# Performance work log

Measured on AMD Instinct MI355X. Metric: run time of the kernel, lower is better.

## Reference

```python
import jax, jax.numpy as jnp
import numpy as np

MODEL_DIM = 1024
NUM_HEADS = 16
D_K = MODEL_DIM // NUM_HEADS  # 64
MAX_SEQ_LEN = 3200
B, T = 2, 2048
THETA_BASE = 10000.0


def setup_inputs() -> dict:
    key = jax.random.key(0)
    ks = jax.random.split(key, 5)
    scale = 1.0 / np.sqrt(MODEL_DIM)
    x = jax.random.normal(ks[0], (B, T, MODEL_DIM), dtype=jnp.float32)
    wq = jax.random.normal(ks[1], (MODEL_DIM, MODEL_DIM), dtype=jnp.float32) * scale
    wk = jax.random.normal(ks[2], (MODEL_DIM, MODEL_DIM), dtype=jnp.float32) * scale
    wv = jax.random.normal(ks[3], (MODEL_DIM, MODEL_DIM), dtype=jnp.float32) * scale
    wo = jax.random.normal(ks[4], (MODEL_DIM, MODEL_DIM), dtype=jnp.float32) * scale
    bq = jnp.zeros((MODEL_DIM,), jnp.float32)
    bk = jnp.zeros((MODEL_DIM,), jnp.float32)
    bv = jnp.zeros((MODEL_DIM,), jnp.float32)
    bo = jnp.zeros((MODEL_DIM,), jnp.float32)
    # RoPE tables, exactly as precompute_rotation_matrix: theta duplicated
    # adjacently ([t0,t0,t1,t1,...]).
    theta = THETA_BASE ** (jnp.arange(D_K // 2, dtype=jnp.float32) * (-2.0 / D_K))
    ang = jnp.outer(jnp.arange(MAX_SEQ_LEN, dtype=jnp.float32), theta)  # [L, d/2]
    ang = jnp.repeat(ang, 2, axis=-1)  # [L, d]
    return {
        "x": x, "wq": wq, "bq": bq, "wk": wk, "bk": bk,
        "wv": wv, "bv": bv, "wo": wo, "bo": bo,
        "cos": jnp.cos(ang), "sin": jnp.sin(ang),
    }


def reference(x, wq, bq, wk, bk, wv, bv, wo, bo, cos, sin):
    b, t, dm = x.shape
    h, d = NUM_HEADS, dm // NUM_HEADS

    # NOTE: original uses .view(b, h, t, d) directly on [b, t, h*d] (no
    # transpose) — a nonstandard head split we replicate faithfully.
    xq = (x @ wq.T + bq).reshape(b, h, t, d)
    xk = (x @ wk.T + bk).reshape(b, h, t, d)
    xv = (x @ wv.T + bv).reshape(b, h, t, d)

    def rot_half(q):
        # pairs are adjacent (2i, 2i+1): out[2i] = -q[2i+1], out[2i+1] = q[2i]
        q2 = q.reshape(b, h, t, d // 2, 2)
        return jnp.stack([-q2[..., 1], q2[..., 0]], axis=-1).reshape(b, h, t, d)

    # NOTE: original indexes cos/sin at the single position `seq_len`
    # (rotation_matrix_cos[:, :, xq.shape[2], :]), broadcasting one row over
    # all positions — replicated faithfully.
    c = cos[t]  # [d]
    s = sin[t]  # [d]
    xq = xq * c + rot_half(xq) * s
    xk = xk * c + rot_half(xk) * s

    scores = jnp.einsum("bhqd,bhkd->bhqk", xq, xk) / np.sqrt(d)
    p = jax.nn.softmax(scores, axis=-1)  # mask='none', dropout=0.0
    o = jnp.einsum("bhqk,bhkd->bhqd", p, xv)
    o = o.transpose(0, 2, 1, 3).reshape(b, t, dm)  # 'b h t d -> b t (h d)'
    return o @ wo.T + bo
```

## Files before the change

### kernel.cpp

```cpp
#include <hip/hip_runtime.h>

typedef _Float16 half8 __attribute__((ext_vector_type(8)));
typedef __fp16 pkh2 __attribute__((ext_vector_type(2)));
typedef float floatx4 __attribute__((ext_vector_type(4)));

#define AS1 __attribute__((address_space(1)))
#define AS3 __attribute__((address_space(3)))


__global__ __launch_bounds__(256) void convert_kernel(
    const float* __restrict__ x, const float* __restrict__ wq,
    const float* __restrict__ wk, const float* __restrict__ wv,
    const float* __restrict__ wo,
    _Float16* __restrict__ xb, _Float16* __restrict__ wqkv,
    _Float16* __restrict__ wob)
{
    int i = (blockIdx.x * 256 + threadIdx.x) * 4;
    const float* src; _Float16* dst; int off;
    if (i < 4194304)      { src = x;  dst = xb;            off = i; }
    else if (i < 5242880) { src = wq; dst = wqkv;          off = i - 4194304; }
    else if (i < 6291456) { src = wk; dst = wqkv + 1048576; off = i - 5242880; }
    else if (i < 7340032) { src = wv; dst = wqkv + 2097152; off = i - 6291456; }
    else                  { src = wo; dst = wob;           off = i - 7340032; }
    float4 v = *(const float4*)(src + off);
    union { uint2 u; pkh2 h[2]; } o;
    o.h[0] = __builtin_amdgcn_cvt_pkrtz(v.x, v.y);
    o.h[1] = __builtin_amdgcn_cvt_pkrtz(v.z, v.w);
    *(uint2*)(dst + off) = o.u;
}

template<bool QKV, int BM, int BN>
__global__ __launch_bounds__(256) void gemm_kernel(
    const _Float16* __restrict__ A, const _Float16* __restrict__ W,
    const float* __restrict__ b0, const float* __restrict__ b1,
    const float* __restrict__ b2,
    const float* __restrict__ cosr, const float* __restrict__ sinr,
    _Float16* __restrict__ O0, _Float16* __restrict__ O1,
    _Float16* __restrict__ O2, float* __restrict__ Of)
{
    constexpr int MT   = (BN == 128) ? BM / 32 : BM / 64;
    constexpr int AISS = BM / 32;
    constexpr int WISS = BN / 32;
    __shared__ __align__(16) _Float16 As[BM * 64];
    __shared__ __align__(16) _Float16 Bs[BN * 64];
    const int tid  = threadIdx.x;
    const int lane = tid & 63, w = tid >> 6;
    const int lrow = lane & 15, quad = lane >> 4;
    const int wr = (BN == 128) ? (w & 1) * (BM / 2) : w * (BM / 4);
    const int wc = (BN == 128) ? (w >> 1) * 64 : 0;

    const int nwg  = gridDim.x * gridDim.y;
    const int flat = blockIdx.y * gridDim.x + blockIdx.x;
    const int idx  = (flat & 7) * (nwg >> 3) + (flat >> 3);
    const int bx   = idx % gridDim.x;
    const int by   = idx / gridDim.x;

    const int arow0 = bx * BM;
    const int brow0 = by * BN;

    const int r8 = lane >> 3;
    const int gcol = ((lane & 7) ^ r8) * 8;

    floatx4 acc[MT][4] = {};

    for (int kk = 0; kk < 1024; kk += 64) {
        __syncthreads();
        for (int u = 0; u < AISS; u++) {
            const int row = w * (8 * AISS) + u * 8;
            __builtin_amdgcn_global_load_lds(
                (const AS1 unsigned*)(const void*)(A + (size_t)(arow0 + row + r8) * 1024 + kk + gcol),
                (AS3 unsigned*)(void*)(As + row * 64), 16, 0, 0);
        }
        for (int u = 0; u < WISS; u++) {
            const int row = w * (8 * WISS) + u * 8;
            __builtin_amdgcn_global_load_lds(
                (const AS1 unsigned*)(const void*)(W + (size_t)(brow0 + row + r8) * 1024 + kk + gcol),
                (AS3 unsigned*)(void*)(Bs + row * 64), 16, 0, 0);
        }
        __syncthreads();
        for (int ks = 0; ks < 2; ks++) {
            const int swz = ((ks * 4 + quad) ^ (lrow & 7)) * 8;
            half8 af[MT], bf[4];
            for (int mt = 0; mt < MT; mt++)
                af[mt] = *(const half8*)&As[(wr + mt * 16 + lrow) * 64 + swz];
            for (int nt = 0; nt < 4; nt++)
                bf[nt] = *(const half8*)&Bs[(wc + nt * 16 + lrow) * 64 + swz];
            for (int mt = 0; mt < MT; mt++)
                for (int nt = 0; nt < 4; nt++)
                    acc[mt][nt] = __builtin_amdgcn_mfma_f32_16x16x32_f16(
                        af[mt], bf[nt], acc[mt][nt], 0, 0, 0);
        }
    }

    if (QKV) {
        constexpr int CTS = 1024 / BN;
        const int seg = by / CTS;
        const float* bias = seg == 0 ? b0 : (seg == 1 ? b1 : b2);
        _Float16* out = seg == 0 ? O0 : (seg == 1 ? O1 : O2);
        const int nbase = (by % CTS) * BN + wc;
        for (int nt = 0; nt < 4; nt++) {
            const int n = nbase + nt * 16 + lrow;
            const float bv = bias[n];
            const int dj = n & 63;
            const float cv = cosr[dj], sv = sinr[dj];
            const bool odd = (n & 1) != 0;
            const int ns = (seg == 1)
                ? ((n & ~56) | ((((n >> 3) ^ (n >> 6)) & 7) << 3))
                : n;
            for (int mt = 0; mt < MT; mt++)
                for (int r = 0; r < 4; r++) {
                    float v = acc[mt][nt][r] + bv;
                    if (seg < 2) {
                        float p = __shfl_xor(v, 1, 64);
                        v = odd ? (v * cv + p * sv) : (v * cv - p * sv);
                    }
                    if (seg == 0) v *= 0.125f;
                    int row = arow0 + wr + mt * 16 + quad * 4 + r;
                    out[row * 1024 + ns] = (_Float16)v;
                }
        }
    } else {
        const int nbase = by * BN + wc;
        for (int nt = 0; nt < 4; nt++) {
            const int n = nbase + nt * 16 + lrow;
            const float bv = b0[n];
            for (int mt = 0; mt < MT; mt++)
                for (int r = 0; r < 4; r++) {
                    int row = arow0 + wr + mt * 16 + quad * 4 + r;
                    Of[row * 1024 + n] = acc[mt][nt][r] + bv;
                }
        }
    }
}

__global__ __launch_bounds__(256) void vtrans_kernel(
    const _Float16* __restrict__ V, _Float16* __restrict__ VT)
{
    __shared__ __align__(16) _Float16 T[64][72];
    const int tid = threadIdx.x;
    const int kt = blockIdx.x;
    const int bh = blockIdx.y;
    const int bi = bh >> 4, hi = bh & 15;
    const _Float16* Vh = V + (size_t)(bi * 2048 + hi * 128) * 1024 + kt * 4096;
    const int srow = tid >> 3, sblk = tid & 7;
    union { uint4 u; _Float16 h[8]; } a, b;
    a.u = *(const uint4*)(Vh + (2 * srow) * 64 + sblk * 8);
    b.u = *(const uint4*)(Vh + (2 * srow + 1) * 64 + sblk * 8);
    for (int j = 0; j < 8; j++) {
        union { unsigned u; _Float16 h[2]; } pk;
        pk.h[0] = a.h[j]; pk.h[1] = b.h[j];
        *(unsigned*)&T[sblk * 8 + j][2 * srow] = pk.u;
    }
    __syncthreads();
    const int d = tid >> 2, c = tid & 3;
    const int xr = d & 7;
    _Float16* outrow = VT + ((size_t)bh * 64 + d) * 2048 + kt * 64;
    *(uint4*)(outrow + ((2 * c)     ^ xr) * 8) = *(const uint4*)&T[d][c * 16];
    *(uint4*)(outrow + ((2 * c + 1) ^ xr) * 8) = *(const uint4*)&T[d][c * 16 + 8];
}

static __device__ __forceinline__ half8 assemble_p(uint2 a, uint2 b) {
    auto s32x = __builtin_amdgcn_permlane32_swap(a.x, b.x, false, false);
    auto s32y = __builtin_amdgcn_permlane32_swap(a.y, b.y, false, false);
    auto s16x = __builtin_amdgcn_permlane16_swap(s32x[0], s32x[1], false, false);
    auto s16y = __builtin_amdgcn_permlane16_swap(s32y[0], s32y[1], false, false);
    union { uint4 u; half8 h; } r;
    r.u.x = s16x[0];
    r.u.y = s16y[0];
    r.u.z = s16x[1];
    r.u.w = s16y[1];
    return r.h;
}

__global__ __launch_bounds__(512, 4) void attn_kernel(
    const _Float16* __restrict__ Q, const _Float16* __restrict__ K,
    const _Float16* __restrict__ VT, _Float16* __restrict__ O)
{
    __shared__ __align__(16) _Float16 smem[32768];

    const int tid  = threadIdx.x;
    const int g    = tid >> 8;
    const int wg   = tid >> 6;
    const int w    = wg & 3;
    const int lane = tid & 63;
    const int lrow = lane & 15, quad = lane >> 4;

    const int bid = blockIdx.x;
    const int bh  = (bid & 7) * 4 + (bid >> 7);
    const int qt  = (bid >> 3) & 15;
    const int bi = bh >> 4, hi = bh & 15;
    const size_t base = (size_t)(bi * 2048 + hi * 128) * 1024;
    const _Float16* Qh  = Q + base;
    const _Float16* Kh  = K + base + (size_t)g * 65536;
    const _Float16* VTh = VT + (size_t)bh * 131072 + g * 1024;

    _Float16* Ks0  = smem + g * 16384;
    _Float16* Vts0 = smem + g * 16384 + 8192;

    half8 qf[2][2];
    for (int nt = 0; nt < 2; nt++)
        for (int ks = 0; ks < 2; ks++)
            qf[nt][ks] = *(const half8*)(Qh + (qt * 128 + w * 32 + nt * 16 + lrow) * 64
                                          + ks * 32 + quad * 8);

    floatx4 oacc[4][2] = {};
    float lsum0 = 0.0f, lsum1 = 0.0f;

    const _Float16* klsrc = Kh + w * 1024 + lane * 8;
    const _Float16* vlsrc = VTh + (size_t)(w * 16 + (lane >> 3)) * 2048 + (lane & 7) * 8;

    auto stage = [&](int kt, int b) {
        const _Float16* ks = klsrc + kt * 4096;
        _Float16* kd = Ks0 + b * 4096 + w * 1024;
        __builtin_amdgcn_global_load_lds((const AS1 unsigned*)(const void*)ks,
                                         (AS3 unsigned*)(void*)kd, 16, 0, 0);
        __builtin_amdgcn_global_load_lds((const AS1 unsigned*)(const void*)(ks + 512),
                                         (AS3 unsigned*)(void*)(kd + 512), 16, 0, 0);
        const _Float16* vs = vlsrc + kt * 64;
        _Float16* vd = Vts0 + b * 4096 + w * 1024;
        __builtin_amdgcn_global_load_lds((const AS1 unsigned*)(const void*)vs,
                                         (AS3 unsigned*)(void*)vd, 16, 0, 0);
        __builtin_amdgcn_global_load_lds((const AS1 unsigned*)(const void*)(vs + 8 * 2048),
                                         (AS3 unsigned*)(void*)(vd + 512), 16, 0, 0);
    };

    const float LOG2E = 1.44269504f;
    const float OFF   = -8.65617025f;

    stage(0, 0);
    __syncthreads();

    for (int ktl = 0; ktl < 16; ktl++) {
        const int cur = ktl & 1;
        if (ktl < 15) stage(ktl + 1, cur ^ 1);
        const _Float16* Ksg  = Ks0 + cur * 4096;
        const _Float16* Vtsg = Vts0 + cur * 4096;
        for (int h = 0; h < 2; h++) {
            union { uint2 u; pkh2 h2[2]; } pA[2], pB[2];
            for (int k2 = 0; k2 < 2; k2++) {
                const int kt4 = h * 2 + k2;
                floatx4 s0 = {}, s1 = {};
                __builtin_amdgcn_s_setprio(1);
                for (int ks = 0; ks < 2; ks++) {
                    half8 af = *(const half8*)&Ksg[(kt4 * 16 + lrow) * 64
                                 + (((ks * 4 + quad) ^ (lrow & 7)) * 8)];
                    s0 = __builtin_amdgcn_mfma_f32_16x16x32_f16(af, qf[0][ks], s0, 0, 0, 0);
                    s1 = __builtin_amdgcn_mfma_f32_16x16x32_f16(af, qf[1][ks], s1, 0, 0, 0);
                }
                __builtin_amdgcn_s_setprio(0);
                float p00 = __builtin_amdgcn_exp2f(fmaf(s0[0], LOG2E, OFF));
                float p01 = __builtin_amdgcn_exp2f(fmaf(s0[1], LOG2E, OFF));
                float p02 = __builtin_amdgcn_exp2f(fmaf(s0[2], LOG2E, OFF));
                float p03 = __builtin_amdgcn_exp2f(fmaf(s0[3], LOG2E, OFF));
                float p10 = __builtin_amdgcn_exp2f(fmaf(s1[0], LOG2E, OFF));
                float p11 = __builtin_amdgcn_exp2f(fmaf(s1[1], LOG2E, OFF));
                float p12 = __builtin_amdgcn_exp2f(fmaf(s1[2], LOG2E, OFF));
                float p13 = __builtin_amdgcn_exp2f(fmaf(s1[3], LOG2E, OFF));
                lsum0 += (p00 + p01) + (p02 + p03);
                lsum1 += (p10 + p11) + (p12 + p13);
                pA[k2].h2[0] = __builtin_amdgcn_cvt_pkrtz(p00, p01);
                pA[k2].h2[1] = __builtin_amdgcn_cvt_pkrtz(p02, p03);
                pB[k2].h2[0] = __builtin_amdgcn_cvt_pkrtz(p10, p11);
                pB[k2].h2[1] = __builtin_amdgcn_cvt_pkrtz(p12, p13);
            }
            half8 bf0 = assemble_p(pA[0].u, pA[1].u);
            half8 bf1 = assemble_p(pB[0].u, pB[1].u);
            __builtin_amdgcn_s_setprio(1);
            for (int dt = 0; dt < 4; dt++) {
                half8 av = *(const half8*)&Vtsg[(dt * 16 + lrow) * 64
                              + (((h * 4 + quad) ^ (lrow & 7)) * 8)];
                oacc[dt][0] = __builtin_amdgcn_mfma_f32_16x16x32_f16(av, bf0, oacc[dt][0], 0, 0, 0);
                oacc[dt][1] = __builtin_amdgcn_mfma_f32_16x16x32_f16(av, bf1, oacc[dt][1], 0, 0, 0);
            }
            __builtin_amdgcn_s_setprio(0);
        }
        __syncthreads();
    }

    float* X = (float*)smem;
    float* L = (float*)(smem + 16384);
    if (g == 1) {
        for (int dt = 0; dt < 4; dt++)
            for (int nt = 0; nt < 2; nt++)
                *(floatx4*)&X[((dt * 2 + nt) * 256 + w * 64 + lane) * 4] = oacc[dt][nt];
        L[(w * 64 + lane) * 2]     = lsum0;
        L[(w * 64 + lane) * 2 + 1] = lsum1;
    }
    __syncthreads();
    if (g == 0) {
        for (int dt = 0; dt < 4; dt++)
            for (int nt = 0; nt < 2; nt++)
                oacc[dt][nt] += *(const floatx4*)&X[((dt * 2 + nt) * 256 + w * 64 + lane) * 4];
        lsum0 += L[(w * 64 + lane) * 2];
        lsum1 += L[(w * 64 + lane) * 2 + 1];
        lsum0 += __shfl_xor(lsum0, 16, 64); lsum0 += __shfl_xor(lsum0, 32, 64);
        lsum1 += __shfl_xor(lsum1, 16, 64); lsum1 += __shfl_xor(lsum1, 32, 64);
        const float inv0 = 1.0f / lsum0, inv1 = 1.0f / lsum1;
        _Float16* Es = smem + 17408 + w * 2304;
        for (int dt = 0; dt < 4; dt++) {
            union { uint2 u; pkh2 h2[2]; } a0, a1;
            a0.h2[0] = __builtin_amdgcn_cvt_pkrtz(oacc[dt][0][0] * inv0, oacc[dt][0][1] * inv0);
            a0.h2[1] = __builtin_amdgcn_cvt_pkrtz(oacc[dt][0][2] * inv0, oacc[dt][0][3] * inv0);
            a1.h2[0] = __builtin_amdgcn_cvt_pkrtz(oacc[dt][1][0] * inv1, oacc[dt][1][1] * inv1);
            a1.h2[1] = __builtin_amdgcn_cvt_pkrtz(oacc[dt][1][2] * inv1, oacc[dt][1][3] * inv1);
            *(uint2*)&Es[lrow * 72 + dt * 16 + quad * 4]        = a0.u;
            *(uint2*)&Es[(16 + lrow) * 72 + dt * 16 + quad * 4] = a1.u;
        }
        const int rw = lane >> 1, hf = lane & 1;
        const size_t orow = (size_t)(bi * 2048 + qt * 128 + w * 32 + rw) * 1024
                            + hi * 64 + hf * 32;
        for (int i = 0; i < 4; i++)
            *(uint4*)(O + orow + i * 8) = *(const uint4*)&Es[rw * 72 + hf * 32 + i * 8];
    }
}

extern "C" void kernel_launch(void* const* d_in, const int* in_sizes, int n_in,
                              void* d_out, int out_size, void* d_ws, size_t ws_size,
                              hipStream_t stream) {
    const float* x    = (const float*)d_in[0];
    const float* wq   = (const float*)d_in[1];
    const float* bq   = (const float*)d_in[2];
    const float* wk   = (const float*)d_in[3];
    const float* bk   = (const float*)d_in[4];
    const float* wv   = (const float*)d_in[5];
    const float* bv   = (const float*)d_in[6];
    const float* wo   = (const float*)d_in[7];
    const float* bo   = (const float*)d_in[8];
    const float* cosT = (const float*)d_in[9];
    const float* sinT = (const float*)d_in[10];

    _Float16* ws   = (_Float16*)d_ws;
    _Float16* xb   = ws;
    _Float16* wqkv = xb + 4194304;
    _Float16* wob  = wqkv + 3145728;
    _Float16* Qb   = wob + 1048576;
    _Float16* Kb   = Qb + 4194304;
    _Float16* Vb   = Kb + 4194304;
    _Float16* Ob   = Vb + 4194304;
    _Float16* VTb  = xb;

    convert_kernel<<<8192, 256, 0, stream>>>(x, wq, wk, wv, wo, xb, wqkv, wob);
    gemm_kernel<true, 64, 64><<<dim3(64, 48), 256, 0, stream>>>(
        xb, wqkv, bq, bk, bv, cosT + 2048 * 64, sinT + 2048 * 64,
        Qb, Kb, Vb, nullptr);
    vtrans_kernel<<<dim3(32, 32), 256, 0, stream>>>(Vb, VTb);
    attn_kernel<<<dim3(512), 512, 0, stream>>>(Qb, Kb, VTb, Ob);
    gemm_kernel<false, 64, 64><<<dim3(64, 16), 256, 0, stream>>>(
        Ob, wob, bo, nullptr, nullptr, nullptr, nullptr,
        nullptr, nullptr, nullptr, (float*)d_out);
}
```

Before: 213.3 us.

## Drop split-K warp groups in attention and enlarge GEMM N tiles

The attention kernel no longer splits the key range across two 256-thread groups. Each 256-thread block now walks all 32 key tiles itself, which removes the shared-memory cross-group reduction and halves LDS use so more blocks fit per CU. Separately, both GEMM launches move to 64x128 tiles with half the grid in N. This trades per-block parallelism and latency hiding for occupancy and less reduction overhead, and the larger GEMM tiles give fewer blocks and possibly more register pressure.

Result: slower. 300.3 us (+40.8%).

```diff
diff --git a/kernel.cpp b/kernel.cpp
--- a/kernel.cpp
+++ b/kernel.cpp
@@ -172,16 +172,14 @@
     return r.h;
 }
 
-__global__ __launch_bounds__(512, 4) void attn_kernel(
+__global__ __launch_bounds__(256, 5) void attn_kernel(
     const _Float16* __restrict__ Q, const _Float16* __restrict__ K,
     const _Float16* __restrict__ VT, _Float16* __restrict__ O)
 {
-    __shared__ __align__(16) _Float16 smem[32768];
+    __shared__ __align__(16) _Float16 smem[16384];
 
     const int tid  = threadIdx.x;
-    const int g    = tid >> 8;
-    const int wg   = tid >> 6;
-    const int w    = wg & 3;
+    const int w    = tid >> 6;
     const int lane = tid & 63;
     const int lrow = lane & 15, quad = lane >> 4;
 
@@ -191,11 +189,11 @@
     const int bi = bh >> 4, hi = bh & 15;
     const size_t base = (size_t)(bi * 2048 + hi * 128) * 1024;
     const _Float16* Qh  = Q + base;
-    const _Float16* Kh  = K + base + (size_t)g * 65536;
-    const _Float16* VTh = VT + (size_t)bh * 131072 + g * 1024;
-
-    _Float16* Ks0  = smem + g * 16384;
-    _Float16* Vts0 = smem + g * 16384 + 8192;
+    const _Float16* Kh  = K + base;
+    const _Float16* VTh = VT + (size_t)bh * 131072;
+
+    _Float16* Ks0  = smem;
+    _Float16* Vts0 = smem + 8192;
 
     half8 qf[2][2];
     for (int nt = 0; nt < 2; nt++)
@@ -230,9 +228,9 @@
     stage(0, 0);
     __syncthreads();
 
-    for (int ktl = 0; ktl < 16; ktl++) {
+    for (int ktl = 0; ktl < 32; ktl++) {
         const int cur = ktl & 1;
-        if (ktl < 15) stage(ktl + 1, cur ^ 1);
+        if (ktl < 31) stage(ktl + 1, cur ^ 1);
         const _Float16* Ksg  = Ks0 + cur * 4096;
         const _Float16* Vtsg = Vts0 + cur * 4096;
         for (int h = 0; h < 2; h++) {
@@ -277,41 +275,24 @@
         __syncthreads();
     }
 
-    float* X = (float*)smem;
-    float* L = (float*)(smem + 16384);
-    if (g == 1) {
-        for (int dt = 0; dt < 4; dt++)
-            for (int nt = 0; nt < 2; nt++)
-                *(floatx4*)&X[((dt * 2 + nt) * 256 + w * 64 + lane) * 4] = oacc[dt][nt];
-        L[(w * 64 + lane) * 2]     = lsum0;
-        L[(w * 64 + lane) * 2 + 1] = lsum1;
-    }
-    __syncthreads();
-    if (g == 0) {
-        for (int dt = 0; dt < 4; dt++)
-            for (int nt = 0; nt < 2; nt++)
-                oacc[dt][nt] += *(const floatx4*)&X[((dt * 2 + nt) * 256 + w * 64 + lane) * 4];
-        lsum0 += L[(w * 64 + lane) * 2];
-        lsum1 += L[(w * 64 + lane) * 2 + 1];
-        lsum0 += __shfl_xor(lsum0, 16, 64); lsum0 += __shfl_xor(lsum0, 32, 64);
-        lsum1 += __shfl_xor(lsum1, 16, 64); lsum1 += __shfl_xor(lsum1, 32, 64);
-        const float inv0 = 1.0f / lsum0, inv1 = 1.0f / lsum1;
-        _Float16* Es = smem + 17408 + w * 2304;
-        for (int dt = 0; dt < 4; dt++) {
-            union { uint2 u; pkh2 h2[2]; } a0, a1;
-            a0.h2[0] = __builtin_amdgcn_cvt_pkrtz(oacc[dt][0][0] * inv0, oacc[dt][0][1] * inv0);
-            a0.h2[1] = __builtin_amdgcn_cvt_pkrtz(oacc[dt][0][2] * inv0, oacc[dt][0][3] * inv0);
-            a1.h2[0] = __builtin_amdgcn_cvt_pkrtz(oacc[dt][1][0] * inv1, oacc[dt][1][1] * inv1);
-            a1.h2[1] = __builtin_amdgcn_cvt_pkrtz(oacc[dt][1][2] * inv1, oacc[dt][1][3] * inv1);
-            *(uint2*)&Es[lrow * 72 + dt * 16 + quad * 4]        = a0.u;
-            *(uint2*)&Es[(16 + lrow) * 72 + dt * 16 + quad * 4] = a1.u;
-        }
-        const int rw = lane >> 1, hf = lane & 1;
-        const size_t orow = (size_t)(bi * 2048 + qt * 128 + w * 32 + rw) * 1024
-                            + hi * 64 + hf * 32;
-        for (int i = 0; i < 4; i++)
-            *(uint4*)(O + orow + i * 8) = *(const uint4*)&Es[rw * 72 + hf * 32 + i * 8];
-    }
+    lsum0 += __shfl_xor(lsum0, 16, 64); lsum0 += __shfl_xor(lsum0, 32, 64);
+    lsum1 += __shfl_xor(lsum1, 16, 64); lsum1 += __shfl_xor(lsum1, 32, 64);
+    const float inv0 = 1.0f / lsum0, inv1 = 1.0f / lsum1;
+    _Float16* Es = smem + w * 2304;
+    for (int dt = 0; dt < 4; dt++) {
+        union { uint2 u; pkh2 h2[2]; } a0, a1;
+        a0.h2[0] = __builtin_amdgcn_cvt_pkrtz(oacc[dt][0][0] * inv0, oacc[dt][0][1] * inv0);
+        a0.h2[1] = __builtin_amdgcn_cvt_pkrtz(oacc[dt][0][2] * inv0, oacc[dt][0][3] * inv0);
+        a1.h2[0] = __builtin_amdgcn_cvt_pkrtz(oacc[dt][1][0] * inv1, oacc[dt][1][1] * inv1);
+        a1.h2[1] = __builtin_amdgcn_cvt_pkrtz(oacc[dt][1][2] * inv1, oacc[dt][1][3] * inv1);
+        *(uint2*)&Es[lrow * 72 + dt * 16 + quad * 4]        = a0.u;
+        *(uint2*)&Es[(16 + lrow) * 72 + dt * 16 + quad * 4] = a1.u;
+    }
+    const int rw = lane >> 1, hf = lane & 1;
+    const size_t orow = (size_t)(bi * 2048 + qt * 128 + w * 32 + rw) * 1024
+                        + hi * 64 + hf * 32;
+    for (int i = 0; i < 4; i++)
+        *(uint4*)(O + orow + i * 8) = *(const uint4*)&Es[rw * 72 + hf * 32 + i * 8];
 }
 
 extern "C" void kernel_launch(void* const* d_in, const int* in_sizes, int n_in,
@@ -340,12 +321,12 @@
     _Float16* VTb  = xb;
 
     convert_kernel<<<8192, 256, 0, stream>>>(x, wq, wk, wv, wo, xb, wqkv, wob);
-    gemm_kernel<true, 64, 64><<<dim3(64, 48), 256, 0, stream>>>(
+    gemm_kernel<true, 64, 128><<<dim3(64, 24), 256, 0, stream>>>(
         xb, wqkv, bq, bk, bv, cosT + 2048 * 64, sinT + 2048 * 64,
         Qb, Kb, Vb, nullptr);
     vtrans_kernel<<<dim3(32, 32), 256, 0, stream>>>(Vb, VTb);
-    attn_kernel<<<dim3(512), 512, 0, stream>>>(Qb, Kb, VTb, Ob);
-    gemm_kernel<false, 64, 64><<<dim3(64, 16), 256, 0, stream>>>(
+    attn_kernel<<<dim3(512), 256, 0, stream>>>(Qb, Kb, VTb, Ob);
+    gemm_kernel<false, 64, 128><<<dim3(64, 8), 256, 0, stream>>>(
         Ob, wob, bo, nullptr, nullptr, nullptr, nullptr,
         nullptr, nullptr, nullptr, (float*)d_out);
 }
```
